# Kernel tuning notes

Measured on AMD Instinct MI355X. Metric: run time of the kernel, lower is better.

Reference implementation:

```python
import jax, jax.numpy as jnp
import numpy as np

KNOWN_POINTS = 8
TAU = 1.0


def setup_inputs() -> dict:
    key = jax.random.key(0)
    k1, k2, k3 = jax.random.split(key, 3)
    B, N, H = 8, 56564, 256
    return {
        "x": jax.random.normal(k1, (B, N), dtype=jnp.float32),
        "point_weight": jax.random.normal(k2, (1, N), dtype=jnp.float32),
        "weight": jax.random.normal(k3, (1, N, H), dtype=jnp.float32),
        "bias": jnp.zeros((1, H), dtype=jnp.float32),
    }


def _softmax_point_selection(point_weight, B, tau):
    """Iterative straight-through HardSoftmax top-k selection (stage=2).
    Returns a (B, N) {0,1}-valued mask (with straight-through softmax grads)."""
    N = point_weight.shape[1]
    weights = jnp.broadcast_to(point_weight, (B, N))  # repeat_interleave over batch
    minimum = jax.lax.stop_gradient(jnp.min(weights))
    total = jnp.zeros((B, N), dtype=weights.dtype)
    for _ in range(KNOWN_POINTS):
        soft = jax.nn.softmax(weights / tau, axis=1)
        hard = jax.nn.one_hot(jnp.argmax(weights, axis=1), N, dtype=weights.dtype)
        # straight-through: forward = hard, backward = softmax jacobian
        one_hot = hard - jax.lax.stop_gradient(soft) + soft
        total = total + one_hot
        # masked_fill at selected positions (no grad through filled entries)
        weights = jnp.where(hard > 0, minimum - 10000.0, weights)
    return total


def reference(x, point_weight, weight, bias):
    B = x.shape[0]
    mask = _softmax_point_selection(point_weight, B, TAU)  # (B, N)
    # out[b,h] = sum_n x[b,n] * mask[b,n] * W[n,h] + bias[h]
    # (equivalent to masking the (B,N,H) weight then matmul, without materializing it)
    out = jnp.einsum('bn,nh->bh', x * mask, weight[0]) + bias
    return out
```

## Files before the change

### kernel.cpp

```cpp
#include <hip/hip_runtime.h>
#include <math.h>

#define TPB 256
#define KSEL 8
#define MAGIC 0x5EEDC0DEu

typedef unsigned long long u64;

__device__ __forceinline__ u64 make_key(float v, unsigned int idx) {
    unsigned int u = __float_as_uint(v);
    unsigned int ord = (u & 0x80000000u) ? ~u : (u | 0x80000000u);
    return ((u64)ord << 32) | (u64)(~idx);
}
__device__ __forceinline__ u64 kmax(u64 a, u64 b) { return a > b ? a : b; }
__device__ __forceinline__ void cswap(u64 &a, u64 &b) {
    u64 hi = a > b ? a : b;
    u64 lo = a > b ? b : a;
    a = hi; b = lo;
}

__device__ __forceinline__ void merge8(u64 a[8], const u64 b[8]) {
    u64 t[8];
    #pragma unroll
    for (int i = 0; i < 8; ++i) t[i] = kmax(a[i], b[7 - i]);
    cswap(t[0], t[4]); cswap(t[1], t[5]); cswap(t[2], t[6]); cswap(t[3], t[7]);
    cswap(t[0], t[2]); cswap(t[1], t[3]); cswap(t[4], t[6]); cswap(t[5], t[7]);
    cswap(t[0], t[1]); cswap(t[2], t[3]); cswap(t[4], t[5]); cswap(t[6], t[7]);
    #pragma unroll
    for (int i = 0; i < 8; ++i) a[i] = t[i];
}

__device__ __forceinline__ void wave_butterfly_top8(u64 r[8]) {
    #pragma unroll
    for (int o = 1; o < 64; o <<= 1) {
        u64 b[8];
        #pragma unroll
        for (int i = 0; i < 8; ++i) b[i] = __shfl_xor(r[i], o, 64);
        merge8(r, b);
    }
}

__global__ __launch_bounds__(TPB) void fused_topk_linear(
        const float* __restrict__ x, const float* __restrict__ pw,
        const float* __restrict__ w, const float* __restrict__ bias,
        float* __restrict__ out,
        unsigned int* __restrict__ flags,
        u64* __restrict__ ws_keys,
        int N, int H, int B, int nblk) {
    __shared__ u64 s_wk[TPB / 64][KSEL];

    const int tid  = threadIdx.x;
    const int lane = tid & 63;
    const int wid  = tid >> 6;
    const int bid  = blockIdx.x;
    const int N4   = N >> 2;
    const int tailN = N - (N4 << 2);
    const int gid  = bid * TPB + tid;

    u64 r[8];
    {
        u64 c0 = 0, c1 = 0, c2 = 0, c3 = 0, c4 = 0;
        if (gid < N4) {
            const float4 v = reinterpret_cast<const float4*>(pw)[gid];
            const unsigned int base = (unsigned int)gid * 4u;
            c0 = make_key(v.x, base + 0u);
            c1 = make_key(v.y, base + 1u);
            c2 = make_key(v.z, base + 2u);
            c3 = make_key(v.w, base + 3u);
        }
        if (bid == 0 && tid < tailN) {
            const unsigned int gi = (unsigned int)(N4 * 4 + tid);
            c4 = make_key(pw[gi], gi);
        }
        cswap(c0, c1); cswap(c3, c4); cswap(c2, c4); cswap(c2, c3); cswap(c0, c3);
        cswap(c0, c2); cswap(c1, c4); cswap(c1, c3); cswap(c1, c2);
        r[0] = c0; r[1] = c1; r[2] = c2; r[3] = c3; r[4] = c4;
        r[5] = 0;  r[6] = 0;  r[7] = 0;
    }

    wave_butterfly_top8(r);

    if (lane == 0) {
        #pragma unroll
        for (int i = 0; i < 8; ++i) s_wk[wid][i] = r[i];
    }
    __syncthreads();
    if (wid == 0) {
        #pragma unroll
        for (int wv = 1; wv < TPB / 64; ++wv) {
            u64 b[8];
            #pragma unroll
            for (int i = 0; i < 8; ++i) b[i] = s_wk[wv][i];
            merge8(r, b);
        }
        if (lane == 0) {
            #pragma unroll
            for (int i = 0; i < 8; ++i)
                __hip_atomic_store(&ws_keys[bid * KSEL + i], r[i],
                                   __ATOMIC_RELAXED, __HIP_MEMORY_SCOPE_AGENT);
            __hip_atomic_store(&flags[bid], MAGIC,
                               __ATOMIC_RELEASE, __HIP_MEMORY_SCOPE_AGENT);
        }
    }
    if (bid >= B) return;

    for (int i = tid; i < nblk; i += TPB) {
        while (__hip_atomic_load(&flags[i], __ATOMIC_ACQUIRE,
                                 __HIP_MEMORY_SCOPE_AGENT) != MAGIC)
            __builtin_amdgcn_s_sleep(1);
    }
    __syncthreads();

    u64 g[8];
    if (lane < nblk) {
        #pragma unroll
        for (int i = 0; i < 8; ++i)
            g[i] = __hip_atomic_load(&ws_keys[lane * KSEL + i],
                                     __ATOMIC_RELAXED, __HIP_MEMORY_SCOPE_AGENT);
    } else {
        #pragma unroll
        for (int i = 0; i < 8; ++i) g[i] = 0ull;
    }
    wave_butterfly_top8(g);

    int idx[KSEL];
    #pragma unroll
    for (int k = 0; k < KSEL; ++k)
        idx[k] = __builtin_amdgcn_readfirstlane((int)(~(unsigned int)(g[k] & 0xffffffffull)));

    const int b = bid;
    float xv[KSEL];
    #pragma unroll
    for (int k = 0; k < KSEL; ++k) xv[k] = x[(size_t)b * N + idx[k]];
    for (int h = tid; h < H; h += TPB) {
        float acc = bias[h];
        #pragma unroll
        for (int k = 0; k < KSEL; ++k) acc += xv[k] * w[(size_t)idx[k] * H + h];
        out[(size_t)b * H + h] = acc;
    }
}

extern "C" void kernel_launch(void* const* d_in, const int* in_sizes, int n_in,
                              void* d_out, int out_size, void* d_ws, size_t ws_size,
                              hipStream_t stream) {
    const float* x    = (const float*)d_in[0];
    const float* pw   = (const float*)d_in[1];
    const float* w    = (const float*)d_in[2];
    const float* bias = (const float*)d_in[3];
    float* out = (float*)d_out;

    const int N = in_sizes[1];
    const int H = in_sizes[3];
    const int B = in_sizes[0] / N;
    const int N4 = N >> 2;
    const int nblk = (N4 + TPB - 1) / TPB;

    unsigned int* flags = (unsigned int*)d_ws;
    u64* keys = (u64*)((char*)d_ws + 512);

    fused_topk_linear<<<nblk, TPB, 0, stream>>>(x, pw, w, bias, out,
                                                flags, keys, N, H, B, nblk);
}
```

Before: 18.61 us.

## Split fused top-k kernel into scan and single-block merge kernels

Replaces the single fused kernel, which used cross-block flag spinning, with two launches. The first uses 64-thread blocks and writes per-block top-8 keys. The second is a single 256-thread block that merges all lists across four waves, then computes every batch row while reusing the loaded weight rows. This removes the spin-wait and flag handshake at the cost of a second kernel launch and a single-block final stage.

New measurement: 17.23 us. 1.08x faster.

```diff
diff --git a/kernel.cpp b/kernel.cpp
--- a/kernel.cpp
+++ b/kernel.cpp
@@ -1,10 +1,7 @@
 #include <hip/hip_runtime.h>
 #include <math.h>
 
-#define TPB 256
 #define KSEL 8
-#define MAGIC 0x5EEDC0DEu
-
 typedef unsigned long long u64;
 
 __device__ __forceinline__ u64 make_key(float v, unsigned int idx) {
@@ -40,103 +37,103 @@
     }
 }
 
-__global__ __launch_bounds__(TPB) void fused_topk_linear(
-        const float* __restrict__ x, const float* __restrict__ pw,
-        const float* __restrict__ w, const float* __restrict__ bias,
-        float* __restrict__ out,
-        unsigned int* __restrict__ flags,
-        u64* __restrict__ ws_keys,
-        int N, int H, int B, int nblk) {
-    __shared__ u64 s_wk[TPB / 64][KSEL];
+__global__ __launch_bounds__(64) void topk_scan(
+        const float* __restrict__ pw, int N, u64* __restrict__ ws_keys) {
+    const int lane = threadIdx.x;
+    const int gid  = blockIdx.x * 64 + lane;
+    const int N4   = N >> 2;
+
+    u64 c0 = 0, c1 = 0, c2 = 0, c3 = 0, c4 = 0;
+    if (gid < N4) {
+        const float4 v = reinterpret_cast<const float4*>(pw)[gid];
+        const unsigned int base = (unsigned int)gid * 4u;
+        c0 = make_key(v.x, base + 0u);
+        c1 = make_key(v.y, base + 1u);
+        c2 = make_key(v.z, base + 2u);
+        c3 = make_key(v.w, base + 3u);
+    }
+    if (blockIdx.x == 0) {
+        int t = N4 * 4 + lane;
+        if (t < N) c4 = make_key(pw[t], (unsigned int)t);
+    }
+    cswap(c0, c1); cswap(c3, c4); cswap(c2, c4); cswap(c2, c3); cswap(c0, c3);
+    cswap(c0, c2); cswap(c1, c4); cswap(c1, c3); cswap(c1, c2);
+
+    u64 r[8] = {c0, c1, c2, c3, c4, 0ull, 0ull, 0ull};
+    wave_butterfly_top8(r);
+
+    if (lane == 0) {
+        #pragma unroll
+        for (int i = 0; i < 8; ++i) ws_keys[blockIdx.x * KSEL + i] = r[i];
+    }
+}
+
+__global__ __launch_bounds__(256) void topk_merge_out(
+        const u64* __restrict__ ws_keys, int nlists,
+        const float* __restrict__ x, const float* __restrict__ w,
+        const float* __restrict__ bias, float* __restrict__ out,
+        int N, int H, int B) {
+    __shared__ u64 s_wk[4][KSEL];
+    __shared__ int s_idx[KSEL];
+    __shared__ float s_x[16][KSEL];
 
     const int tid  = threadIdx.x;
     const int lane = tid & 63;
     const int wid  = tid >> 6;
-    const int bid  = blockIdx.x;
-    const int N4   = N >> 2;
-    const int tailN = N - (N4 << 2);
-    const int gid  = bid * TPB + tid;
 
-    u64 r[8];
-    {
-        u64 c0 = 0, c1 = 0, c2 = 0, c3 = 0, c4 = 0;
-        if (gid < N4) {
-            const float4 v = reinterpret_cast<const float4*>(pw)[gid];
-            const unsigned int base = (unsigned int)gid * 4u;
-            c0 = make_key(v.x, base + 0u);
-            c1 = make_key(v.y, base + 1u);
-            c2 = make_key(v.z, base + 2u);
-            c3 = make_key(v.w, base + 3u);
-        }
-        if (bid == 0 && tid < tailN) {
-            const unsigned int gi = (unsigned int)(N4 * 4 + tid);
-            c4 = make_key(pw[gi], gi);
-        }
-        cswap(c0, c1); cswap(c3, c4); cswap(c2, c4); cswap(c2, c3); cswap(c0, c3);
-        cswap(c0, c2); cswap(c1, c4); cswap(c1, c3); cswap(c1, c2);
-        r[0] = c0; r[1] = c1; r[2] = c2; r[3] = c3; r[4] = c4;
-        r[5] = 0;  r[6] = 0;  r[7] = 0;
+    const int per = (nlists + 3) >> 2;
+    const int li  = wid * per + lane;
+    u64 g[8] = {0ull, 0ull, 0ull, 0ull, 0ull, 0ull, 0ull, 0ull};
+    if (lane < per && li < nlists) {
+        #pragma unroll
+        for (int i = 0; i < 8; ++i) g[i] = ws_keys[li * KSEL + i];
     }
-
-    wave_butterfly_top8(r);
-
+    wave_butterfly_top8(g);
     if (lane == 0) {
         #pragma unroll
-        for (int i = 0; i < 8; ++i) s_wk[wid][i] = r[i];
+        for (int i = 0; i < 8; ++i) s_wk[wid][i] = g[i];
     }
     __syncthreads();
+
     if (wid == 0) {
+        u64 a[8], b[8];
         #pragma unroll
-        for (int wv = 1; wv < TPB / 64; ++wv) {
-            u64 b[8];
+        for (int i = 0; i < 8; ++i) a[i] = s_wk[0][i];
+        #pragma unroll
+        for (int wv = 1; wv < 4; ++wv) {
             #pragma unroll
             for (int i = 0; i < 8; ++i) b[i] = s_wk[wv][i];
-            merge8(r, b);
+            merge8(a, b);
         }
         if (lane == 0) {
             #pragma unroll
-            for (int i = 0; i < 8; ++i)
-                __hip_atomic_store(&ws_keys[bid * KSEL + i], r[i],
-                                   __ATOMIC_RELAXED, __HIP_MEMORY_SCOPE_AGENT);
-            __hip_atomic_store(&flags[bid], MAGIC,
-                               __ATOMIC_RELEASE, __HIP_MEMORY_SCOPE_AGENT);
+            for (int k = 0; k < KSEL; ++k)
+                s_idx[k] = (int)(~(unsigned int)(a[k] & 0xffffffffull));
         }
-    }
-    if (bid >= B) return;
-
-    for (int i = tid; i < nblk; i += TPB) {
-        while (__hip_atomic_load(&flags[i], __ATOMIC_ACQUIRE,
-                                 __HIP_MEMORY_SCOPE_AGENT) != MAGIC)
-            __builtin_amdgcn_s_sleep(1);
     }
     __syncthreads();
 
-    u64 g[8];
-    if (lane < nblk) {
-        #pragma unroll
-        for (int i = 0; i < 8; ++i)
-            g[i] = __hip_atomic_load(&ws_keys[lane * KSEL + i],
-                                     __ATOMIC_RELAXED, __HIP_MEMORY_SCOPE_AGENT);
-    } else {
-        #pragma unroll
-        for (int i = 0; i < 8; ++i) g[i] = 0ull;
-    }
-    wave_butterfly_top8(g);
-
     int idx[KSEL];
     #pragma unroll
-    for (int k = 0; k < KSEL; ++k)
-        idx[k] = __builtin_amdgcn_readfirstlane((int)(~(unsigned int)(g[k] & 0xffffffffull)));
+    for (int k = 0; k < KSEL; ++k) idx[k] = s_idx[k];
 
-    const int b = bid;
-    float xv[KSEL];
-    #pragma unroll
-    for (int k = 0; k < KSEL; ++k) xv[k] = x[(size_t)b * N + idx[k]];
-    for (int h = tid; h < H; h += TPB) {
-        float acc = bias[h];
+    if (tid < B * KSEL) {
+        const int b = tid >> 3, k = tid & 7;
+        s_x[b][k] = x[(size_t)b * N + idx[k]];
+    }
+    __syncthreads();
+
+    for (int h = tid; h < H; h += 256) {
+        float wv[KSEL];
         #pragma unroll
-        for (int k = 0; k < KSEL; ++k) acc += xv[k] * w[(size_t)idx[k] * H + h];
-        out[(size_t)b * H + h] = acc;
+        for (int k = 0; k < KSEL; ++k) wv[k] = w[(size_t)idx[k] * H + h];
+        const float bv = bias[h];
+        for (int b = 0; b < B; ++b) {
+            float acc = bv;
+            #pragma unroll
+            for (int k = 0; k < KSEL; ++k) acc += s_x[b][k] * wv[k];
+            out[(size_t)b * H + h] = acc;
+        }
     }
 }
 
@@ -153,11 +150,10 @@
     const int H = in_sizes[3];
     const int B = in_sizes[0] / N;
     const int N4 = N >> 2;
-    const int nblk = (N4 + TPB - 1) / TPB;
+    const int nblk = (N4 + 63) / 64;
 
-    unsigned int* flags = (unsigned int*)d_ws;
-    u64* keys = (u64*)((char*)d_ws + 512);
+    u64* keys = (u64*)d_ws;
 
-    fused_topk_linear<<<nblk, TPB, 0, stream>>>(x, pw, w, bias, out,
-                                                flags, keys, N, H, B, nblk);
+    topk_scan<<<nblk, 64, 0, stream>>>(pw, N, keys);
+    topk_merge_out<<<1, 256, 0, stream>>>(keys, nblk, x, w, bias, out, N, H, B);
 }
```
